# Performance work log

Hardware: AMD Instinct MI355X
Metric: run time of the kernel (lower is better)

## Reference

```python
import jax, jax.numpy as jnp
import numpy as np

N, NODE_DIM, EDGE_DIM, MSG_DIM, T = 1024, 128, 16, 64, 3
IN_DIM = 2 * NODE_DIM + EDGE_DIM


def setup_inputs() -> dict:
    key = jax.random.key(0)
    ks = jax.random.split(key, 11)
    s = 0.05
    X = jax.random.normal(ks[0], (N, NODE_DIM), jnp.float32)
    A = jax.random.randint(ks[1], (N, N), 0, 2, jnp.int32)  # 0/1 adjacency
    E = jax.random.normal(ks[2], (N, N, EDGE_DIM), jnp.float32)
    # MessageFn MLP params (torch Linear: y = x @ W.T + b)
    W1 = jax.random.normal(ks[3], (MSG_DIM, IN_DIM), jnp.float32) * s
    b1 = jax.random.normal(ks[4], (MSG_DIM,), jnp.float32) * s
    W2 = jax.random.normal(ks[5], (MSG_DIM, MSG_DIM), jnp.float32) * s
    b2 = jax.random.normal(ks[6], (MSG_DIM,), jnp.float32) * s
    # GRUCell params (torch layout: [r|z|n] stacked along rows)
    W_ih = jax.random.normal(ks[7], (3 * NODE_DIM, MSG_DIM), jnp.float32) * s
    b_ih = jax.random.normal(ks[8], (3 * NODE_DIM,), jnp.float32) * s
    W_hh = jax.random.normal(ks[9], (3 * NODE_DIM, NODE_DIM), jnp.float32) * s
    b_hh = jax.random.normal(ks[10], (3 * NODE_DIM,), jnp.float32) * s
    return {"X": X, "A": A, "E": E, "W1": W1, "b1": b1, "W2": W2, "b2": b2,
            "W_ih": W_ih, "b_ih": b_ih, "W_hh": W_hh, "b_hh": b_hh}


def reference(X, A, E, W1, b1, W2, b2, W_ih, b_ih, W_hh, b_hh):
    Amask = A.astype(X.dtype)  # (N, N) 0/1
    # Split first Linear over the concat [h_i, h_j, e_ij]
    Wi = W1[:, :NODE_DIM]
    Wj = W1[:, NODE_DIM:2 * NODE_DIM]
    We = W1[:, 2 * NODE_DIM:]
    # Edge contribution is constant over the T steps: (N, N, msg)
    Ep = jnp.einsum('ije,me->ijm', E, We)
    H = X
    for _ in range(T):
        hi = H @ Wi.T  # (N, msg) -- destination-node contribution
        hj = H @ Wj.T  # (N, msg) -- source-node contribution
        pre = hi[:, None, :] + hj[None, :, :] + Ep + b1  # (N, N, msg)
        msg = jax.nn.relu(pre) @ W2.T + b2               # (N, N, msg)
        # Masked sum over neighbors j (zero vector if no neighbors)
        M = jnp.einsum('ij,ijm->im', Amask, msg)          # (N, msg)
        # GRUCell: h' = (1-z)*n + z*h
        gi = M @ W_ih.T + b_ih
        gh = H @ W_hh.T + b_hh
        gi_r, gi_z, gi_n = jnp.split(gi, 3, axis=-1)
        gh_r, gh_z, gh_n = jnp.split(gh, 3, axis=-1)
        r = jax.nn.sigmoid(gi_r + gh_r)
        z = jax.nn.sigmoid(gi_z + gh_z)
        n = jnp.tanh(gi_n + r * gh_n)
        H = (1.0 - z) * n + z * H
    return H
```

## Files before the change

kernel.cpp:

```cpp
#include <hip/hip_runtime.h>
#include <cstddef>

#define N 1024
#define DN 128
#define DE 16
#define DM 64
#define TSTEPS 3
#define INDIM 272

__global__ __launch_bounds__(512, 4) void kInit(const float* __restrict__ H,
                                                const float* __restrict__ W1,
                                                const float* __restrict__ W_hh,
                                                const float* __restrict__ b_hh,
                                                float* __restrict__ P) {
  int i = blockIdx.x;
  int t = threadIdx.x;
  __shared__ float h[DN];
  if (t < DN) h[t] = H[(size_t)i * DN + t];
  __syncthreads();

  const float* w;
  float acc;
  if (t < 64)       { w = W1 + (size_t)t * INDIM;              acc = 0.f; }
  else if (t < 128) { w = W1 + (size_t)(t - 64) * INDIM + 128; acc = 0.f; }
  else              { w = W_hh + (size_t)(t - 128) * DN;       acc = b_hh[t - 128]; }
  const float4* w4 = (const float4*)w;
  float a0 = 0.f, a1 = 0.f;
  #pragma unroll
  for (int k4 = 0; k4 < DN / 8; ++k4) {
    float4 wv0 = w4[2 * k4];
    float4 wv1 = w4[2 * k4 + 1];
    a0 = fmaf(h[k4 * 8 + 0], wv0.x, a0);
    a1 = fmaf(h[k4 * 8 + 4], wv1.x, a1);
    a0 = fmaf(h[k4 * 8 + 1], wv0.y, a0);
    a1 = fmaf(h[k4 * 8 + 5], wv1.y, a1);
    a0 = fmaf(h[k4 * 8 + 2], wv0.z, a0);
    a1 = fmaf(h[k4 * 8 + 6], wv1.z, a1);
    a0 = fmaf(h[k4 * 8 + 3], wv0.w, a0);
    a1 = fmaf(h[k4 * 8 + 7], wv1.w, a1);
  }
  P[(size_t)i * 512 + t] = acc + a0 + a1;
}

__global__ __launch_bounds__(512, 4) void kStep(const float* __restrict__ Pcur,
                                                const float* __restrict__ E,
                                                const float* __restrict__ W1,
                                                const float* __restrict__ b1,
                                                const int* __restrict__ A,
                                                const float* __restrict__ W2,
                                                const float* __restrict__ b2,
                                                const float* __restrict__ W_ih,
                                                const float* __restrict__ b_ih,
                                                const float* __restrict__ W_hh,
                                                const float* __restrict__ b_hh,
                                                const float* __restrict__ Hin,
                                                float* __restrict__ Hout,
                                                float* __restrict__ Pnext,
                                                int doPA) {
  int i  = blockIdx.x;
  int t  = threadIdx.x;
  int m  = t & 63;
  int jg = t >> 6;

  __shared__ int   sA[N];
  __shared__ float red[8][DM];
  __shared__ float dred[8];
  __shared__ float sS[DM];
  __shared__ float sM[DM];
  __shared__ float sGi[384];
  __shared__ float sH[DN];
  __shared__ float sdeg;

  const int* Arow = A + (size_t)i * N;
  sA[t]       = Arow[t];
  sA[t + 512] = Arow[t + 512];

  float we[16];
  {
    const float4* wr4 = (const float4*)(W1 + (size_t)m * INDIM + 256);
    #pragma unroll
    for (int q = 0; q < 4; ++q) {
      float4 v = wr4[q];
      we[q * 4 + 0] = v.x;
      we[q * 4 + 1] = v.y;
      we[q * 4 + 2] = v.z;
      we[q * 4 + 3] = v.w;
    }
  }
  float hib = Pcur[(size_t)i * 512 + m] + b1[m];

  __syncthreads();

  float s = 0.f;
  int   dg = 0;

  const float4* e4  = (const float4*)(E + ((size_t)i * N + jg) * DE);
  const float*  hjp = Pcur + (size_t)jg * 512 + 64 + m;

  #pragma unroll 2
  for (int jt = 0; jt < N / 8; ++jt) {
    float4 q0 = e4[0], q1 = e4[1], q2 = e4[2], q3 = e4[3];
    float  hj = *hjp;
    int    a  = sA[jt * 8 + jg];
    if (m == 0) dg += a;

    float acc = hib + hj;
    acc = fmaf(q0.x, we[0],  acc);
    acc = fmaf(q0.y, we[1],  acc);
    acc = fmaf(q0.z, we[2],  acc);
    acc = fmaf(q0.w, we[3],  acc);
    acc = fmaf(q1.x, we[4],  acc);
    acc = fmaf(q1.y, we[5],  acc);
    acc = fmaf(q1.z, we[6],  acc);
    acc = fmaf(q1.w, we[7],  acc);
    acc = fmaf(q2.x, we[8],  acc);
    acc = fmaf(q2.y, we[9],  acc);
    acc = fmaf(q2.z, we[10], acc);
    acc = fmaf(q2.w, we[11], acc);
    acc = fmaf(q3.x, we[12], acc);
    acc = fmaf(q3.y, we[13], acc);
    acc = fmaf(q3.z, we[14], acc);
    acc = fmaf(q3.w, we[15], acc);

    s = fmaf((float)a, fmaxf(acc, 0.f), s);

    e4  += 8 * DE / 4;
    hjp += 8 * 512;
  }

  red[jg][m] = s;
  if (m == 0) dred[jg] = (float)dg;
  __syncthreads();

  if (t < DM) {
    float acc = 0.f;
    #pragma unroll
    for (int r = 0; r < 8; ++r) acc += red[r][t];
    sS[t] = acc;
  }
  if (t == DM) {
    float d = 0.f;
    #pragma unroll
    for (int r = 0; r < 8; ++r) d += dred[r];
    sdeg = d;
  }
  __syncthreads();

  if (t < DM) {
    float acc = sdeg * b2[t];
    const float4* w4 = (const float4*)(W2 + (size_t)t * DM);
    #pragma unroll
    for (int k4 = 0; k4 < DM / 4; ++k4) {
      float4 wv = w4[k4];
      acc = fmaf(sS[k4 * 4 + 0], wv.x, acc);
      acc = fmaf(sS[k4 * 4 + 1], wv.y, acc);
      acc = fmaf(sS[k4 * 4 + 2], wv.z, acc);
      acc = fmaf(sS[k4 * 4 + 3], wv.w, acc);
    }
    sM[t] = acc;
  }
  __syncthreads();

  if (t < 384) {
    float acc = b_ih[t];
    const float4* w4 = (const float4*)(W_ih + (size_t)t * DM);
    #pragma unroll
    for (int k4 = 0; k4 < DM / 4; ++k4) {
      float4 wv = w4[k4];
      acc = fmaf(sM[k4 * 4 + 0], wv.x, acc);
      acc = fmaf(sM[k4 * 4 + 1], wv.y, acc);
      acc = fmaf(sM[k4 * 4 + 2], wv.z, acc);
      acc = fmaf(sM[k4 * 4 + 3], wv.w, acc);
    }
    sGi[t] = acc;
  }
  __syncthreads();

  if (t < DN) {
    float ghr = Pcur[(size_t)i * 512 + 128 + t];
    float ghz = Pcur[(size_t)i * 512 + 256 + t];
    float ghn = Pcur[(size_t)i * 512 + 384 + t];
    float gir = sGi[t], giz = sGi[128 + t], gin = sGi[256 + t];
    float r = 1.f / (1.f + expf(-(gir + ghr)));
    float z = 1.f / (1.f + expf(-(giz + ghz)));
    float n = tanhf(gin + r * ghn);
    float h = Hin[(size_t)i * DN + t];
    float hn = (1.f - z) * n + z * h;
    sH[t] = hn;
    Hout[(size_t)i * DN + t] = hn;
  }
  __syncthreads();

  if (doPA) {
    const float* w;
    float acc;
    if (t < 64)       { w = W1 + (size_t)t * INDIM;              acc = 0.f; }
    else if (t < 128) { w = W1 + (size_t)(t - 64) * INDIM + 128; acc = 0.f; }
    else              { w = W_hh + (size_t)(t - 128) * DN;       acc = b_hh[t - 128]; }
    const float4* w4 = (const float4*)w;
    float a0 = 0.f, a1 = 0.f;
    #pragma unroll
    for (int k4 = 0; k4 < DN / 8; ++k4) {
      float4 wv0 = w4[2 * k4];
      float4 wv1 = w4[2 * k4 + 1];
      a0 = fmaf(sH[k4 * 8 + 0], wv0.x, a0);
      a1 = fmaf(sH[k4 * 8 + 4], wv1.x, a1);
      a0 = fmaf(sH[k4 * 8 + 1], wv0.y, a0);
      a1 = fmaf(sH[k4 * 8 + 5], wv1.y, a1);
      a0 = fmaf(sH[k4 * 8 + 2], wv0.z, a0);
      a1 = fmaf(sH[k4 * 8 + 6], wv1.z, a1);
      a0 = fmaf(sH[k4 * 8 + 3], wv0.w, a0);
      a1 = fmaf(sH[k4 * 8 + 7], wv1.w, a1);
    }
    Pnext[(size_t)i * 512 + t] = acc + a0 + a1;
  }
}

extern "C" void kernel_launch(void* const* d_in, const int* in_sizes, int n_in,
                              void* d_out, int out_size, void* d_ws, size_t ws_size,
                              hipStream_t stream) {
  const float* X    = (const float*)d_in[0];
  const int*   A    = (const int*)  d_in[1];
  const float* E    = (const float*)d_in[2];
  const float* W1   = (const float*)d_in[3];
  const float* b1   = (const float*)d_in[4];
  const float* W2   = (const float*)d_in[5];
  const float* b2   = (const float*)d_in[6];
  const float* W_ih = (const float*)d_in[7];
  const float* b_ih = (const float*)d_in[8];
  const float* W_hh = (const float*)d_in[9];
  const float* b_hh = (const float*)d_in[10];
  float* out = (float*)d_out;

  float* ws   = (float*)d_ws;
  float* Hbuf = ws;
  float* P0   = Hbuf + N * DN;
  float* P1   = P0 + N * 512;

  kInit<<<N, 512, 0, stream>>>(X, W1, W_hh, b_hh, P0);

  const float* Hin = X;
  float* Pc = P0;
  float* Pn = P1;
  for (int step = 0; step < TSTEPS; ++step) {
    int last = (step == TSTEPS - 1);
    float* Hout = last ? out : Hbuf;
    kStep<<<N, 512, 0, stream>>>(Pc, E, W1, b1, A, W2, b2, W_ih, b_ih,
                                 W_hh, b_hh, Hin, Hout, Pn, last ? 0 : 1);
    Hin = Hbuf;
    float* tmp = Pc; Pc = Pn; Pn = tmp;
  }
}
```

Measured before the change: 611.6 us.

## Compact neighbor lists per row and skip non-edges with double-buffered edge staging

Each block now ballots over its adjacency row to build a compacted list of neighbor indices, so the message loop visits only actual edges and skips roughly half the work on a random 0/1 adjacency. Edge features for the next 64 neighbors are gathered into a double-buffered shared tile while the current tile is computed, and the block size drops from 512 to 256 threads, with the GRU and projection stages looping over outputs. This trades coalesced streaming of E for gathered loads, adds prefix-scan and synchronisation overhead, and computes padded slots that are then masked out.

```diff
diff --git a/kernel.cpp b/kernel.cpp
--- a/kernel.cpp
+++ b/kernel.cpp
@@ -1,5 +1,6 @@
 #include <hip/hip_runtime.h>
 #include <cstddef>
+#include <cstdint>
 
 #define N 1024
 #define DN 128
@@ -42,7 +43,7 @@
   P[(size_t)i * 512 + t] = acc + a0 + a1;
 }
 
-__global__ __launch_bounds__(512, 4) void kStep(const float* __restrict__ Pcur,
+__global__ __launch_bounds__(256, 4) void kStep(const float* __restrict__ Pcur,
                                                 const float* __restrict__ E,
                                                 const float* __restrict__ W1,
                                                 const float* __restrict__ b1,
@@ -57,27 +58,56 @@
                                                 float* __restrict__ Hout,
                                                 float* __restrict__ Pnext,
                                                 int doPA) {
-  int i  = blockIdx.x;
-  int t  = threadIdx.x;
-  int m  = t & 63;
-  int jg = t >> 6;
-
-  __shared__ int   sA[N];
-  __shared__ float red[8][DM];
-  __shared__ float dred[8];
+  int i    = blockIdx.x;
+  int t    = threadIdx.x;
+  int lane = t & 63;
+  int w    = t >> 6;
+
+  __shared__ int   sList[N];
+  __shared__ float sE[2][64 * DE];
+  __shared__ int   sCnt[16];
+  __shared__ int   sBase[16];
+  __shared__ int   sDeg;
+  __shared__ float red[4][DM];
   __shared__ float sS[DM];
   __shared__ float sM[DM];
   __shared__ float sGi[384];
   __shared__ float sH[DN];
-  __shared__ float sdeg;
 
   const int* Arow = A + (size_t)i * N;
-  sA[t]       = Arow[t];
-  sA[t + 512] = Arow[t + 512];
+  uint64_t lmask = (lane == 0) ? 0ull : ((~0ull) >> (64 - lane));
+  int myj[4], mypre[4], myact[4];
+  #pragma unroll
+  for (int r = 0; r < 4; ++r) {
+    int j = r * 256 + t;
+    int a = Arow[j];
+    uint64_t mask = __ballot(a != 0);
+    myj[r]   = j;
+    myact[r] = a;
+    mypre[r] = __popcll(mask & lmask);
+    if (lane == 0) sCnt[r * 4 + w] = __popcll(mask);
+  }
+  __syncthreads();
+  if (t == 0) {
+    int acc = 0;
+    #pragma unroll
+    for (int s = 0; s < 16; ++s) { sBase[s] = acc; acc += sCnt[s]; }
+    sDeg = acc;
+  }
+  __syncthreads();
+  #pragma unroll
+  for (int r = 0; r < 4; ++r)
+    if (myact[r]) sList[sBase[r * 4 + w] + mypre[r]] = myj[r];
+  __syncthreads();
+  int deg    = sDeg;
+  int ntiles = (deg + 63) >> 6;
+  int padded = ntiles << 6;
+  if (t < padded - deg) sList[deg + t] = 0;
+  __syncthreads();
 
   float we[16];
   {
-    const float4* wr4 = (const float4*)(W1 + (size_t)m * INDIM + 256);
+    const float4* wr4 = (const float4*)(W1 + (size_t)lane * INDIM + 256);
     #pragma unroll
     for (int q = 0; q < 4; ++q) {
       float4 v = wr4[q];
@@ -87,67 +117,78 @@
       we[q * 4 + 3] = v.w;
     }
   }
-  float hib = Pcur[(size_t)i * 512 + m] + b1[m];
-
+  float hib = Pcur[(size_t)i * 512 + lane] + b1[lane];
+
+  int sl2 = (w << 4) + (lane >> 2);
+  int ch4 = (lane & 3) * 4;
+  const float* Ebase = E + (size_t)i * N * DE;
+
+  if (ntiles > 0) {
+    int jv = sList[sl2];
+    float4 ge = *(const float4*)(Ebase + (size_t)jv * DE + ch4);
+    *(float4*)&sE[0][sl2 * DE + ch4] = ge;
+  }
   __syncthreads();
 
   float s = 0.f;
-  int   dg = 0;
-
-  const float4* e4  = (const float4*)(E + ((size_t)i * N + jg) * DE);
-  const float*  hjp = Pcur + (size_t)jg * 512 + 64 + m;
-
-  #pragma unroll 2
-  for (int jt = 0; jt < N / 8; ++jt) {
-    float4 q0 = e4[0], q1 = e4[1], q2 = e4[2], q3 = e4[3];
-    float  hj = *hjp;
-    int    a  = sA[jt * 8 + jg];
-    if (m == 0) dg += a;
-
-    float acc = hib + hj;
-    acc = fmaf(q0.x, we[0],  acc);
-    acc = fmaf(q0.y, we[1],  acc);
-    acc = fmaf(q0.z, we[2],  acc);
-    acc = fmaf(q0.w, we[3],  acc);
-    acc = fmaf(q1.x, we[4],  acc);
-    acc = fmaf(q1.y, we[5],  acc);
-    acc = fmaf(q1.z, we[6],  acc);
-    acc = fmaf(q1.w, we[7],  acc);
-    acc = fmaf(q2.x, we[8],  acc);
-    acc = fmaf(q2.y, we[9],  acc);
-    acc = fmaf(q2.z, we[10], acc);
-    acc = fmaf(q2.w, we[11], acc);
-    acc = fmaf(q3.x, we[12], acc);
-    acc = fmaf(q3.y, we[13], acc);
-    acc = fmaf(q3.z, we[14], acc);
-    acc = fmaf(q3.w, we[15], acc);
-
-    s = fmaf((float)a, fmaxf(acc, 0.f), s);
-
-    e4  += 8 * DE / 4;
-    hjp += 8 * 512;
-  }
-
-  red[jg][m] = s;
-  if (m == 0) dred[jg] = (float)dg;
-  __syncthreads();
-
+  int buf = 0;
+  for (int T = 0; T < ntiles; ++T) {
+    int sb = (T << 6) + (w << 4);
+
+    float hj[16];
+    #pragma unroll
+    for (int k = 0; k < 16; ++k) {
+      int jv = sList[sb + k];
+      hj[k] = Pcur[(size_t)jv * 512 + 64 + lane];
+    }
+
+    float4 ge;
+    bool doStage = (T + 1 < ntiles);
+    if (doStage) {
+      int jv2 = sList[((T + 1) << 6) + sl2];
+      ge = *(const float4*)(Ebase + (size_t)jv2 * DE + ch4);
+    }
+
+    const float* eb = &sE[buf][(w << 4) * DE];
+    #pragma unroll
+    for (int k = 0; k < 16; ++k) {
+      float acc = hib + hj[k];
+      const float* ep = eb + k * DE;
+      acc = fmaf(ep[0],  we[0],  acc);
+      acc = fmaf(ep[1],  we[1],  acc);
+      acc = fmaf(ep[2],  we[2],  acc);
+      acc = fmaf(ep[3],  we[3],  acc);
+      acc = fmaf(ep[4],  we[4],  acc);
+      acc = fmaf(ep[5],  we[5],  acc);
+      acc = fmaf(ep[6],  we[6],  acc);
+      acc = fmaf(ep[7],  we[7],  acc);
+      acc = fmaf(ep[8],  we[8],  acc);
+      acc = fmaf(ep[9],  we[9],  acc);
+      acc = fmaf(ep[10], we[10], acc);
+      acc = fmaf(ep[11], we[11], acc);
+      acc = fmaf(ep[12], we[12], acc);
+      acc = fmaf(ep[13], we[13], acc);
+      acc = fmaf(ep[14], we[14], acc);
+      acc = fmaf(ep[15], we[15], acc);
+      float wt = (sb + k < deg) ? 1.f : 0.f;
+      s = fmaf(wt, fmaxf(acc, 0.f), s);
+    }
+
+    if (doStage) *(float4*)&sE[buf ^ 1][sl2 * DE + ch4] = ge;
+    __syncthreads();
+    buf ^= 1;
+  }
+
+  red[w][lane] = s;
+  __syncthreads();
   if (t < DM) {
-    float acc = 0.f;
-    #pragma unroll
-    for (int r = 0; r < 8; ++r) acc += red[r][t];
+    float acc = red[0][t] + red[1][t] + red[2][t] + red[3][t];
     sS[t] = acc;
   }
-  if (t == DM) {
-    float d = 0.f;
-    #pragma unroll
-    for (int r = 0; r < 8; ++r) d += dred[r];
-    sdeg = d;
-  }
   __syncthreads();
 
   if (t < DM) {
-    float acc = sdeg * b2[t];
+    float acc = (float)deg * b2[t];
     const float4* w4 = (const float4*)(W2 + (size_t)t * DM);
     #pragma unroll
     for (int k4 = 0; k4 < DM / 4; ++k4) {
@@ -161,9 +202,9 @@
   }
   __syncthreads();
 
-  if (t < 384) {
-    float acc = b_ih[t];
-    const float4* w4 = (const float4*)(W_ih + (size_t)t * DM);
+  for (int c = t; c < 384; c += 256) {
+    float acc = b_ih[c];
+    const float4* w4 = (const float4*)(W_ih + (size_t)c * DM);
     #pragma unroll
     for (int k4 = 0; k4 < DM / 4; ++k4) {
       float4 wv = w4[k4];
@@ -172,7 +213,7 @@
       acc = fmaf(sM[k4 * 4 + 2], wv.z, acc);
       acc = fmaf(sM[k4 * 4 + 3], wv.w, acc);
     }
-    sGi[t] = acc;
+    sGi[c] = acc;
   }
   __syncthreads();
 
@@ -192,27 +233,29 @@
   __syncthreads();
 
   if (doPA) {
-    const float* w;
-    float acc;
-    if (t < 64)       { w = W1 + (size_t)t * INDIM;              acc = 0.f; }
-    else if (t < 128) { w = W1 + (size_t)(t - 64) * INDIM + 128; acc = 0.f; }
-    else              { w = W_hh + (size_t)(t - 128) * DN;       acc = b_hh[t - 128]; }
-    const float4* w4 = (const float4*)w;
-    float a0 = 0.f, a1 = 0.f;
-    #pragma unroll
-    for (int k4 = 0; k4 < DN / 8; ++k4) {
-      float4 wv0 = w4[2 * k4];
-      float4 wv1 = w4[2 * k4 + 1];
-      a0 = fmaf(sH[k4 * 8 + 0], wv0.x, a0);
-      a1 = fmaf(sH[k4 * 8 + 4], wv1.x, a1);
-      a0 = fmaf(sH[k4 * 8 + 1], wv0.y, a0);
-      a1 = fmaf(sH[k4 * 8 + 5], wv1.y, a1);
-      a0 = fmaf(sH[k4 * 8 + 2], wv0.z, a0);
-      a1 = fmaf(sH[k4 * 8 + 6], wv1.z, a1);
-      a0 = fmaf(sH[k4 * 8 + 3], wv0.w, a0);
-      a1 = fmaf(sH[k4 * 8 + 7], wv1.w, a1);
-    }
-    Pnext[(size_t)i * 512 + t] = acc + a0 + a1;
+    for (int c = t; c < 512; c += 256) {
+      const float* wp;
+      float acc;
+      if (c < 64)       { wp = W1 + (size_t)c * INDIM;              acc = 0.f; }
+      else if (c < 128) { wp = W1 + (size_t)(c - 64) * INDIM + 128; acc = 0.f; }
+      else              { wp = W_hh + (size_t)(c - 128) * DN;       acc = b_hh[c - 128]; }
+      const float4* w4 = (const float4*)wp;
+      float a0 = 0.f, a1 = 0.f;
+      #pragma unroll
+      for (int k4 = 0; k4 < DN / 8; ++k4) {
+        float4 wv0 = w4[2 * k4];
+        float4 wv1 = w4[2 * k4 + 1];
+        a0 = fmaf(sH[k4 * 8 + 0], wv0.x, a0);
+        a1 = fmaf(sH[k4 * 8 + 4], wv1.x, a1);
+        a0 = fmaf(sH[k4 * 8 + 1], wv0.y, a0);
+        a1 = fmaf(sH[k4 * 8 + 5], wv1.y, a1);
+        a0 = fmaf(sH[k4 * 8 + 2], wv0.z, a0);
+        a1 = fmaf(sH[k4 * 8 + 6], wv1.z, a1);
+        a0 = fmaf(sH[k4 * 8 + 3], wv0.w, a0);
+        a1 = fmaf(sH[k4 * 8 + 7], wv1.w, a1);
+      }
+      Pnext[(size_t)i * 512 + c] = acc + a0 + a1;
+    }
   }
 }
 
@@ -245,7 +288,7 @@
   for (int step = 0; step < TSTEPS; ++step) {
     int last = (step == TSTEPS - 1);
     float* Hout = last ? out : Hbuf;
-    kStep<<<N, 512, 0, stream>>>(Pc, E, W1, b1, A, W2, b2, W_ih, b_ih,
+    kStep<<<N, 256, 0, stream>>>(Pc, E, W1, b1, A, W2, b2, W_ih, b_ih,
                                  W_hh, b_hh, Hin, Hout, Pn, last ? 0 : 1);
     Hin = Hbuf;
     float* tmp = Pc; Pc = Pn; Pn = tmp;
```

Measured after the change: 1.810 ms. 196% more time.
